# Optimization experiments

Measured on AMD Instinct MI355X. Metric: run time of the kernel, lower is better.

## Reference

```python
import jax, jax.numpy as jnp
import numpy as np

B, L, H, TE = 256, 2048, 64, 64  # batch, seq len, hidden_size, num_time_enc_dims


def _lin_init(k, out_d, in_d):
    bound = 1.0 / np.sqrt(in_d)
    kw, kb = jax.random.split(k)
    w = jax.random.uniform(kw, (out_d, in_d), jnp.float32, -bound, bound)
    b = jax.random.uniform(kb, (out_d,), jnp.float32, -bound, bound)
    return w, b


def setup_inputs() -> dict:
    key = jax.random.key(0)
    ks = jax.random.split(key, 16)
    x_xy = jax.random.normal(ks[0], (B, L, 2), jnp.float32)
    mask = jax.random.bernoulli(ks[1], 0.8, (B, L, 1)).astype(jnp.float32)  # 0 => masked position
    x = jnp.concatenate([x_xy, mask], axis=-1)  # (B,L,3)
    t = jax.random.uniform(ks[2], (B, L, 1), jnp.float32)
    te_w1, te_b1 = _lin_init(ks[3], TE, 1)
    te_w2, te_b2 = _lin_init(ks[4], TE, TE)
    fproj_w, fproj_b = _lin_init(ks[5], H, 3 + TE)
    bproj_w, bproj_b = _lin_init(ks[6], H, 3 + TE)
    fwz, fbz = _lin_init(ks[7], H, H)
    fwh, fbh = _lin_init(ks[8], H, H)
    bwz, bbz = _lin_init(ks[9], H, H)
    bwh, bbh = _lin_init(ks[10], H, H)
    head_hidden = max((2 * H + TE) // 2, 128)  # = 128
    gh_w1, gh_b1 = _lin_init(ks[11], head_hidden, 2 * H + TE)
    gh_w2, gh_b2 = _lin_init(ks[12], 1, head_hidden)
    mask_token = jnp.array([0.0, 0.01], jnp.float32) + jnp.array([0.1, 0.001], jnp.float32) * jax.random.normal(ks[13], (2,), jnp.float32)
    return dict(x=x, t=t, mask_token=mask_token,
                te_w1=te_w1, te_b1=te_b1, te_w2=te_w2, te_b2=te_b2,
                fproj_w=fproj_w, fproj_b=fproj_b, bproj_w=bproj_w, bproj_b=bproj_b,
                fwz=fwz, fbz=fbz, fwh=fwh, fbh=fbh,
                bwz=bwz, bbz=bbz, bwh=bwh, bbh=bbh,
                gh_w1=gh_w1, gh_b1=gh_b1, gh_w2=gh_w2, gh_b2=gh_b2)


def _mingru_prestates(inp, wz, bz, wh, bh, reverse):
    # inp: (B,L,H). Returns the hidden state BEFORE each step's update, in
    # time order, matching the torch code which stores h_* before cell.step.
    z = jax.nn.sigmoid(jnp.einsum('blh,oh->blo', inp, wz) + bz)
    h_tilde = jnp.tanh(jnp.einsum('blh,oh->blo', inp, wh) + bh)

    def step(h, zh):
        z_t, ht_t = zh
        return (1.0 - z_t) * h + z_t * ht_t, h  # emit pre-update carry

    h0 = jnp.zeros((inp.shape[0], wz.shape[0]), inp.dtype)
    _, hs = jax.lax.scan(step, h0,
                         (jnp.swapaxes(z, 0, 1), jnp.swapaxes(h_tilde, 0, 1)),
                         reverse=reverse)
    return jnp.swapaxes(hs, 0, 1)  # (B,L,H)


def reference(x, t, mask_token,
              te_w1, te_b1, te_w2, te_b2,
              fproj_w, fproj_b, bproj_w, bproj_b,
              fwz, fbz, fwh, fbh,
              bwz, bbz, bwh, bbh,
              gh_w1, gh_b1, gh_w2, gh_b2):
    mask_chan = x[..., 2:3]                      # (B,L,1)
    masked_pos = mask_chan == 0
    x_first2 = jnp.where(masked_pos, mask_token.reshape(1, 1, 2), x[..., :2])
    x3 = jnp.concatenate([x_first2, mask_chan], axis=-1)  # (B,L,3)

    t_enc = jax.nn.relu(jnp.einsum('blk,ok->blo', t, te_w1) + te_b1)
    t_enc = jnp.einsum('blk,ok->blo', t_enc, te_w2) + te_b2  # (B,L,TE)

    x_cat = jnp.concatenate([x3, t_enc], axis=-1)  # (B,L,3+TE)

    inp_fwd = jnp.einsum('blk,ok->blo', x_cat, fproj_w) + fproj_b
    inp_bwd = jnp.einsum('blk,ok->blo', x_cat, bproj_w) + bproj_b

    h_fwd = _mingru_prestates(inp_fwd, fwz, fbz, fwh, fbh, reverse=False)  # state after steps 0..t-1
    h_bwd = _mingru_prestates(inp_bwd, bwz, bbz, bwh, bbh, reverse=True)   # state after steps L-1..t+1

    h_fwd_final = h_fwd[:, -1:, :]  # state after steps 0..L-2
    h_bwd_final = h_bwd[:, 0:1, :]  # state after steps L-1..1

    unmasked = mask_chan > 0
    h_fwd_apply = jnp.where(unmasked, h_fwd, h_fwd_final)
    h_bwd_apply = jnp.where(unmasked, h_bwd, h_bwd_final)

    h_bi = jnp.concatenate([h_fwd_apply, h_bwd_apply, t_enc], axis=-1)  # (B,L,2H+TE)
    hid = jax.nn.relu(jnp.einsum('blk,ok->blo', h_bi, gh_w1) + gh_b1)
    preds = jnp.einsum('blk,ok->blo', hid, gh_w2) + gh_b2  # (B,L,1)
    return preds
```

## Files before the change

### kernel.cpp

```cpp
#include <hip/hip_runtime.h>
#include <stdint.h>

#define NB 256
#define NL 2048

typedef __attribute__((ext_vector_type(8))) short short8;
typedef __attribute__((ext_vector_type(4))) float f32x4;
#define MFMA16(a,b,c) __builtin_amdgcn_mfma_f32_16x16x32_bf16(a,b,c,0,0,0)

static __device__ __forceinline__ unsigned short f2bf(float f) {
    union { float f; uint32_t u; } v; v.f = f;
    uint32_t u = v.u;
    uint32_t r = u + 0x7fffu + ((u >> 16) & 1u);
    return (unsigned short)(r >> 16);
}
static __device__ __forceinline__ float bflo(uint32_t u) {
    union { uint32_t u; float f; } v; v.u = u << 16; return v.f;
}
static __device__ __forceinline__ float bfhi(uint32_t u) {
    union { uint32_t u; float f; } v; v.u = u & 0xffff0000u; return v.f;
}
#if __has_builtin(__builtin_amdgcn_cvt_pk_bf16_f32)
typedef __attribute__((ext_vector_type(2))) __bf16 bf16x2_t;
static __device__ __forceinline__ uint32_t pk2(float lo, float hi) {
    union { bf16x2_t v; uint32_t u; } c;
    c.v = __builtin_amdgcn_cvt_pk_bf16_f32(lo, hi);
    return c.u;
}
static __device__ __forceinline__ unsigned short bf1(float v) {
    union { bf16x2_t v; uint32_t u; } c;
    c.v = __builtin_amdgcn_cvt_pk_bf16_f32(v, v);
    return (unsigned short)(c.u & 0xffffu);
}
#else
static __device__ __forceinline__ uint32_t pk2(float lo, float hi) {
    return ((uint32_t)f2bf(hi) << 16) | (uint32_t)f2bf(lo);
}
static __device__ __forceinline__ unsigned short bf1(float v) { return f2bf(v); }
#endif
static __device__ __forceinline__ short8 frag8(const float* p) {
    short8 r;
#pragma unroll
    for (int j = 0; j < 8; ++j) r[j] = (short)f2bf(p[j]);
    return r;
}

static __device__ __forceinline__ void barrier_lds() {
    asm volatile("s_waitcnt lgkmcnt(0)" ::: "memory");
    __builtin_amdgcn_s_barrier();
}

#define SSTR 129

__global__ __launch_bounds__(512) void scan_fused(
    const float* __restrict__ x, const float* __restrict__ t,
    const float* __restrict__ mtok,
    const float* __restrict__ te_w1, const float* __restrict__ te_b1,
    const float* __restrict__ te_w2, const float* __restrict__ te_b2,
    const float* __restrict__ fpw, const float* __restrict__ fpb,
    const float* __restrict__ bpw, const float* __restrict__ bpb,
    const float* __restrict__ fwz, const float* __restrict__ fbz,
    const float* __restrict__ fwh, const float* __restrict__ fbh,
    const float* __restrict__ bwz, const float* __restrict__ bbz,
    const float* __restrict__ bwh, const float* __restrict__ bbh,
    int b0,
    unsigned short* __restrict__ hf, unsigned short* __restrict__ hb)
{
    __shared__ __align__(16) unsigned short s_tenc[128*72];
    __shared__ __align__(16) unsigned short s_inp[128*72];
    __shared__ uint32_t s_seg[64*SSTR];
    __shared__ float s_A[8][65], s_B[8][65];
    __shared__ float s_H[64];
    __shared__ float2 s_wb[64];

    const int rl  = blockIdx.x >> 1;
    const int dir = blockIdx.x & 1;
    const int tid = threadIdx.x;
    const int h   = tid & 63;
    const int q   = tid >> 6;
    const int lq  = h >> 4;
    const int ln  = h & 15;
    const int mq  = q >> 1;
    const int nh  = q & 1;

    const int gx = (b0 + rl) << 11;
    unsigned short* out = (dir ? hb : hf) + (size_t)rl * NL * 64;

    short8 bte[2][2];
    float bite[2];
#pragma unroll
    for (int ni = 0; ni < 2; ++ni) {
        const int nt = nh*2 + ni;
        const float* row = te_w2 + (nt*16 + ln)*64;
#pragma unroll
        for (int ks = 0; ks < 2; ++ks) bte[ni][ks] = frag8(row + lq*8 + ks*32);
        bite[ni] = te_b2[nt*16 + ln];
    }
    const float* PW = dir ? bpw : fpw;
    const float* PB = dir ? bpb : fpb;
    short8 bpj[2][3];
    float bipj[2];
#pragma unroll
    for (int ni = 0; ni < 2; ++ni) {
        const int nt = nh*2 + ni;
        const float* row = PW + (nt*16 + ln)*67;
#pragma unroll
        for (int ks = 0; ks < 2; ++ks) {
            float tmp[8];
#pragma unroll
            for (int j = 0; j < 8; ++j) tmp[j] = row[3 + lq*8 + ks*32 + j];
            bpj[ni][ks] = frag8(tmp);
        }
        {
            float tmp[8];
#pragma unroll
            for (int j = 0; j < 8; ++j) tmp[j] = (lq == 0 && j < 3) ? row[j] : 0.f;
            bpj[ni][2] = frag8(tmp);
        }
        bipj[ni] = PB[nt*16 + ln];
    }
    const float* WZ = dir ? bwz : fwz;
    const float* WH = dir ? bwh : fwh;
    const float* BZ = dir ? bbz : fbz;
    const float* BH = dir ? bbh : fbh;
    short8 bz[2][2], bh[2][2];
    float biz[2], bih[2];
#pragma unroll
    for (int ni = 0; ni < 2; ++ni) {
        const int nt = nh*2 + ni;
        const float* rz = WZ + (nt*16 + ln)*64;
        const float* rh = WH + (nt*16 + ln)*64;
#pragma unroll
        for (int ks = 0; ks < 2; ++ks) {
            bz[ni][ks] = frag8(rz + lq*8 + ks*32);
            bh[ni][ks] = frag8(rh + lq*8 + ks*32);
        }
        biz[ni] = BZ[nt*16 + ln];
        bih[ni] = BH[nt*16 + ln];
    }
    const float mt0 = mtok[0], mt1 = mtok[1];

    auto G1 = [&](const float* tvv) {
#pragma unroll
        for (int mi = 0; mi < 2; ++mi) {
            short8 a0, a1;
#pragma unroll
            for (int j = 0; j < 8; ++j) {
                const float2 wb0 = s_wb[lq*8 + j];
                const float2 wb1 = s_wb[lq*8 + 32 + j];
                a0[j] = (short)bf1(fmaxf(fmaf(tvv[mi], wb0.x, wb0.y), 0.f));
                a1[j] = (short)bf1(fmaxf(fmaf(tvv[mi], wb1.x, wb1.y), 0.f));
            }
#pragma unroll
            for (int ni = 0; ni < 2; ++ni) {
                f32x4 c = {0.f, 0.f, 0.f, 0.f};
                c = MFMA16(a0, bte[ni][0], c);
                c = MFMA16(a1, bte[ni][1], c);
                const int o = (nh*2+ni)*16 + ln;
#pragma unroll
                for (int r = 0; r < 4; ++r)
                    s_tenc[((mq*2+mi)*16 + lq*4 + r)*72 + o] = bf1(c[r] + bite[ni]);
            }
        }
    };
    auto G2 = [&](const float* xr0_, const float* xr1_, const float* xmc_) {
#pragma unroll
        for (int mi = 0; mi < 2; ++mi) {
            const int mrow = (mq*2+mi)*16 + ln;
            const short8 a0 = *(const short8*)(s_tenc + mrow*72 + lq*8);
            const short8 a1 = *(const short8*)(s_tenc + mrow*72 + lq*8 + 32);
            short8 a2 = {0,0,0,0,0,0,0,0};
            if (lq == 0) {
                const float mc  = xmc_[mi];
                const float x0m = (mc == 0.f) ? mt0 : xr0_[mi];
                const float x1m = (mc == 0.f) ? mt1 : xr1_[mi];
                a2[0] = (short)bf1(x0m);
                a2[1] = (short)bf1(x1m);
                a2[2] = (short)bf1(mc);
            }
#pragma unroll
            for (int ni = 0; ni < 2; ++ni) {
                f32x4 c = {0.f, 0.f, 0.f, 0.f};
                c = MFMA16(a0, bpj[ni][0], c);
                c = MFMA16(a1, bpj[ni][1], c);
                c = MFMA16(a2, bpj[ni][2], c);
                const int o = (nh*2+ni)*16 + ln;
#pragma unroll
                for (int r = 0; r < 4; ++r)
                    s_inp[((mq*2+mi)*16 + lq*4 + r)*72 + o] = bf1(c[r] + bipj[ni]);
            }
        }
    };
    auto GATES = [&]() {
#pragma unroll
        for (int mi = 0; mi < 2; ++mi) {
            const int mrow = (mq*2+mi)*16 + ln;
            const short8 a0 = *(const short8*)(s_inp + mrow*72 + lq*8);
            const short8 a1 = *(const short8*)(s_inp + mrow*72 + lq*8 + 32);
#pragma unroll
            for (int ni = 0; ni < 2; ++ni) {
                f32x4 cz  = {0.f, 0.f, 0.f, 0.f};
                f32x4 ch2 = {0.f, 0.f, 0.f, 0.f};
                cz  = MFMA16(a0, bz[ni][0], cz);
                cz  = MFMA16(a1, bz[ni][1], cz);
                ch2 = MFMA16(a0, bh[ni][0], ch2);
                ch2 = MFMA16(a1, bh[ni][1], ch2);
                const int hcol = (nh*2+ni)*16 + ln;
#pragma unroll
                for (int r = 0; r < 4; ++r) {
                    const float az = cz[r]  + biz[ni];
                    const float ah = ch2[r] + bih[ni];
                    const float z  = __builtin_amdgcn_rcpf(1.f + __expf(-az));
                    const float cc = fminf(fmaxf(ah, -15.f), 15.f);
                    const float e2 = __expf(2.f * cc);
                    const float th = 1.f - 2.f * __builtin_amdgcn_rcpf(e2 + 1.f);
                    s_seg[hcol*SSTR + (mq*2+mi)*16 + lq*4 + r] = pk2(1.f - z, z * th);
                }
            }
        }
    };

    if (tid < 64) {
        s_H[tid] = 0.f;
        s_wb[tid] = make_float2(te_w1[tid], te_b1[tid]);
    }
    barrier_lds();

    const int s0 = dir ? 15 : 0;
    {
        float tv0[2];
#pragma unroll
        for (int mi = 0; mi < 2; ++mi)
            tv0[mi] = t[gx + s0*128 + (mq*2+mi)*16 + ln];
        G1(tv0);
    }
    barrier_lds();
    {
        float xr0_[2], xr1_[2], xmc_[2];
        if (lq == 0) {
#pragma unroll
            for (int mi = 0; mi < 2; ++mi) {
                const float* xp = x + (size_t)(gx + s0*128 + (mq*2+mi)*16 + ln)*3;
                xr0_[mi] = xp[0]; xr1_[mi] = xp[1]; xmc_[mi] = xp[2];
            }
        }
        G2(xr0_, xr1_, xmc_);
    }
    barrier_lds();

    uint32_t regs[16];
    int l0p = 0;

#pragma unroll 1
    for (int si = 0; si < 16; ++si) {
        const int s = dir ? (15 - si) : si;
        const int sn = dir ? (14 - si) : (si + 1);
        if (si > 0) {
            float hv = s_A[q][h];
#pragma unroll
            for (int i = 0; i < 16; ++i) {
                const int g = q*16 + i;
                const int xx = dir ? (127 - g) : g;
                out[(size_t)(l0p + xx)*64 + h] = bf1(hv);
                hv = fmaf(bflo(regs[i]), hv, bfhi(regs[i]));
            }
        }
        GATES();
        barrier_lds();
        float tvn[2];
        if (si < 15) {
#pragma unroll
            for (int mi = 0; mi < 2; ++mi)
                tvn[mi] = t[gx + sn*128 + (mq*2+mi)*16 + ln];
        }
        {
            float A = 1.f, Bc = 0.f;
#pragma unroll
            for (int i = 0; i < 16; ++i) {
                const int g = q*16 + i;
                const int xx = dir ? (127 - g) : g;
                const uint32_t uab = s_seg[h*SSTR + xx];
                regs[i] = uab;
                Bc = fmaf(bflo(uab), Bc, bfhi(uab));
                A *= bflo(uab);
            }
            s_A[q][h] = A; s_B[q][h] = Bc;
        }
        if (si < 15) G1(tvn);
        barrier_lds();
        float xr0_[2], xr1_[2], xmc_[2];
        if (si < 15 && lq == 0) {
#pragma unroll
            for (int mi = 0; mi < 2; ++mi) {
                const float* xp = x + (size_t)(gx + sn*128 + (mq*2+mi)*16 + ln)*3;
                xr0_[mi] = xp[0]; xr1_[mi] = xp[1]; xmc_[mi] = xp[2];
            }
        }
        if (tid < 64) {
            float H = s_H[tid];
#pragma unroll
            for (int qq = 0; qq < 8; ++qq) {
                const float a = s_A[qq][tid], b = s_B[qq][tid];
                s_A[qq][tid] = H;
                H = fmaf(a, H, b);
            }
            s_H[tid] = H;
        }
        if (si < 15) G2(xr0_, xr1_, xmc_);
        barrier_lds();
        l0p = s * 128;
    }
    {
        float hv = s_A[q][h];
#pragma unroll
        for (int i = 0; i < 16; ++i) {
            const int g = q*16 + i;
            const int xx = dir ? (127 - g) : g;
            out[(size_t)(l0p + xx)*64 + h] = bf1(hv);
            hv = fmaf(bflo(regs[i]), hv, bfhi(regs[i]));
        }
    }
}

__global__ __launch_bounds__(256, 3) void head_kernel(
    const float* __restrict__ x, const float* __restrict__ t,
    const float* __restrict__ te_w1, const float* __restrict__ te_b1,
    const float* __restrict__ te_w2, const float* __restrict__ te_b2,
    const unsigned short* __restrict__ hf, const unsigned short* __restrict__ hb,
    const float* __restrict__ w1, const float* __restrict__ b1,
    const float* __restrict__ w2, const float* __restrict__ b2,
    int b0,
    float* __restrict__ out)
{
    __shared__ __align__(16) unsigned short s_a[64*200];
    __shared__ __align__(16) unsigned short s_te1[64*72];
    __shared__ float s_part[4][64];
    __shared__ float s_mc[64];

    const int tid = threadIdx.x;
    const int w   = tid >> 6;
    const int l   = tid & 63;
    const int lq  = l >> 4;
    const int ln  = l & 15;

    short8 bw1[2][6];
    float b1v[2], w2v[2];
#pragma unroll
    for (int p = 0; p < 2; ++p) {
        const int o = (2*w + p)*16 + ln;
        const float* row = w1 + o*192;
#pragma unroll
        for (int ks = 0; ks < 6; ++ks) bw1[p][ks] = frag8(row + lq*8 + ks*32);
        b1v[p] = b1[o];
        w2v[p] = w2[o];
    }
    short8 bte[2];
    {
        const float* row = te_w2 + (w*16 + ln)*64;
#pragma unroll
        for (int ks = 0; ks < 2; ++ks) bte[ks] = frag8(row + lq*8 + ks*32);
    }
    const float bias_te = te_b2[w*16 + ln];
    const float bias2 = b2[0];

    const int baseposl = blockIdx.x * 256;

    auto A = [&](int ch) {
        const int gbase = (b0 << 11) + baseposl + ch*64;
        if (tid < 64) s_mc[tid] = x[(size_t)(gbase + tid)*3 + 2];
        const int pos = tid & 63;
        const float tv = t[gbase + pos];
        const int k0 = (tid >> 6) * 16;
        uint32_t* dst = (uint32_t*)(s_te1 + pos*72 + k0);
#pragma unroll
        for (int kk = 0; kk < 16; kk += 2) {
            float v0 = fmaxf(fmaf(tv, te_w1[k0+kk],   te_b1[k0+kk]),   0.f);
            float v1 = fmaxf(fmaf(tv, te_w1[k0+kk+1], te_b1[k0+kk+1]), 0.f);
            dst[kk >> 1] = pk2(v0, v1);
        }
    };
    auto Bp = [&](int ch) {
        const int chbase = baseposl + ch*64;
        const int ll0 = chbase & 2047;
        const int bl  = chbase >> 11;
        const size_t rowbase = (size_t)bl * NL * 64;
#pragma unroll
        for (int rep = 0; rep < 4; ++rep) {
            const int idx = rep*256 + tid;
            const int seg = idx >> 9;
            const int row = (idx >> 3) & 63;
            const int c   = idx & 7;
            const bool unm = s_mc[row] > 0.f;
            const uint4* src = (seg == 0)
                ? (const uint4*)(hf + rowbase + (size_t)(unm ? (ll0+row) : (NL-1))*64)
                : (const uint4*)(hb + rowbase + (size_t)(unm ? (ll0+row) : 0)*64);
            ((uint4*)s_a)[row*25 + seg*8 + c] = src[c];
        }
        const int o = w*16 + ln;
#pragma unroll
        for (int mt = 0; mt < 4; ++mt) {
            f32x4 c = {0.f, 0.f, 0.f, 0.f};
#pragma unroll
            for (int ks = 0; ks < 2; ++ks) {
                const short8 a = *(const short8*)(s_te1 + (mt*16+ln)*72 + lq*8 + ks*32);
                c = MFMA16(a, bte[ks], c);
            }
#pragma unroll
            for (int r = 0; r < 4; ++r) {
                const int m = mt*16 + lq*4 + r;
                s_a[m*200 + 128 + o] = bf1(c[r] + bias_te);
            }
        }
    };
    auto Cp = [&]() {
#pragma unroll
        for (int mt = 0; mt < 4; ++mt) {
            short8 af[6];
#pragma unroll
            for (int ks = 0; ks < 6; ++ks)
                af[ks] = *(const short8*)(s_a + (mt*16+ln)*200 + lq*8 + ks*32);
            float vs[4] = {0.f, 0.f, 0.f, 0.f};
#pragma unroll
            for (int p = 0; p < 2; ++p) {
                f32x4 c = {0.f, 0.f, 0.f, 0.f};
#pragma unroll
                for (int ks = 0; ks < 6; ++ks) c = MFMA16(af[ks], bw1[p][ks], c);
#pragma unroll
                for (int r = 0; r < 4; ++r)
                    vs[r] += fmaxf(c[r] + b1v[p], 0.f) * w2v[p];
            }
#pragma unroll
            for (int mask = 1; mask < 16; mask <<= 1) {
#pragma unroll
                for (int r = 0; r < 4; ++r)
                    vs[r] += __shfl_xor(vs[r], mask);
            }
            if (ln == 0) {
#pragma unroll
                for (int r = 0; r < 4; ++r)
                    s_part[w][mt*16 + lq*4 + r] = vs[r];
            }
        }
    };
    auto Dp = [&](int ch) {
        const int gbase = (b0 << 11) + baseposl + ch*64;
        if (tid < 64) {
            out[gbase + tid] = s_part[0][tid] + s_part[1][tid]
                             + s_part[2][tid] + s_part[3][tid] + bias2;
        }
    };

    A(0);
    barrier_lds();
#pragma unroll 1
    for (int ch = 0; ch < 4; ++ch) {
        Bp(ch);
        barrier_lds();
        Cp();
        barrier_lds();
        Dp(ch);
        if (ch < 3) A(ch + 1);
        barrier_lds();
    }
}

extern "C" void kernel_launch(void* const* d_in, const int* in_sizes, int n_in,
                              void* d_out, int out_size, void* d_ws, size_t ws_size,
                              hipStream_t stream)
{
    const float* x     = (const float*)d_in[0];
    const float* t     = (const float*)d_in[1];
    const float* mtok  = (const float*)d_in[2];
    const float* te_w1 = (const float*)d_in[3];
    const float* te_b1 = (const float*)d_in[4];
    const float* te_w2 = (const float*)d_in[5];
    const float* te_b2 = (const float*)d_in[6];
    const float* fpw   = (const float*)d_in[7];
    const float* fpb   = (const float*)d_in[8];
    const float* bpw   = (const float*)d_in[9];
    const float* bpb   = (const float*)d_in[10];
    const float* fwz   = (const float*)d_in[11];
    const float* fbz   = (const float*)d_in[12];
    const float* fwh   = (const float*)d_in[13];
    const float* fbh   = (const float*)d_in[14];
    const float* bwz   = (const float*)d_in[15];
    const float* bbz   = (const float*)d_in[16];
    const float* bwh   = (const float*)d_in[17];
    const float* bbh   = (const float*)d_in[18];
    const float* w1    = (const float*)d_in[19];
    const float* b1    = (const float*)d_in[20];
    const float* w2    = (const float*)d_in[21];
    const float* b2    = (const float*)d_in[22];

    const size_t per_b = 524288ull;
    int Bg = NB;
    while ((size_t)Bg * per_b > ws_size && Bg > 1) Bg >>= 1;
    const int nG = NB / Bg;

    char* ws = (char*)d_ws;
    unsigned short* hf = (unsigned short*)ws;
    unsigned short* hb = hf + (size_t)Bg * NL * 64;

    for (int g = 0; g < nG; ++g) {
        const int b0 = g * Bg;

        scan_fused<<<2 * Bg, 512, 0, stream>>>(
            x, t, mtok, te_w1, te_b1, te_w2, te_b2,
            fpw, fpb, bpw, bpb, fwz, fbz, fwh, fbh, bwz, bbz, bwh, bbh,
            b0, hf, hb);

        head_kernel<<<8 * Bg, 256, 0, stream>>>(
            x, t, te_w1, te_b1, te_w2, te_b2,
            hf, hb, w1, b1, w2, b2, b0, (float*)d_out);
    }
}
```

Baseline: 323.0 us.

## Prefetch next chunk's hidden states into registers during head MLP compute

The head kernel now issues global loads of the next chunk's forward/backward hidden states into registers before running the MLP on the current chunk, and writes them to LDS only after that compute. The time-encoding first layer is computed directly in registers as MFMA A-fragments, so the s_te1 LDS staging buffer goes away. The mask channel for all four chunks is loaded once up front, and the per-iteration barrier count drops from three to two. The cost is more register pressure from holding prefetched uint4s, which could hurt occupancy under the launch_bounds(256,3) constraint.

After: 336.3 us. +4.1%, slower.

```diff
diff --git a/kernel.cpp b/kernel.cpp
--- a/kernel.cpp
+++ b/kernel.cpp
@@ -333,9 +333,9 @@
     float* __restrict__ out)
 {
     __shared__ __align__(16) unsigned short s_a[64*200];
-    __shared__ __align__(16) unsigned short s_te1[64*72];
     __shared__ float s_part[4][64];
-    __shared__ float s_mc[64];
+    __shared__ float s_mcall[256];
+    __shared__ float2 s_wb[64];
 
     const int tid = threadIdx.x;
     const int w   = tid >> 6;
@@ -364,22 +364,11 @@
     const float bias2 = b2[0];
 
     const int baseposl = blockIdx.x * 256;
-
-    auto A = [&](int ch) {
-        const int gbase = (b0 << 11) + baseposl + ch*64;
-        if (tid < 64) s_mc[tid] = x[(size_t)(gbase + tid)*3 + 2];
-        const int pos = tid & 63;
-        const float tv = t[gbase + pos];
-        const int k0 = (tid >> 6) * 16;
-        uint32_t* dst = (uint32_t*)(s_te1 + pos*72 + k0);
-#pragma unroll
-        for (int kk = 0; kk < 16; kk += 2) {
-            float v0 = fmaxf(fmaf(tv, te_w1[k0+kk],   te_b1[k0+kk]),   0.f);
-            float v1 = fmaxf(fmaf(tv, te_w1[k0+kk+1], te_b1[k0+kk+1]), 0.f);
-            dst[kk >> 1] = pk2(v0, v1);
-        }
-    };
-    auto Bp = [&](int ch) {
+    const int gbase0 = (b0 << 11) + baseposl;
+
+    uint4 greg[4];
+
+    auto GISSUE = [&](int ch) {
         const int chbase = baseposl + ch*64;
         const int ll0 = chbase & 2047;
         const int bl  = chbase >> 11;
@@ -390,26 +379,43 @@
             const int seg = idx >> 9;
             const int row = (idx >> 3) & 63;
             const int c   = idx & 7;
-            const bool unm = s_mc[row] > 0.f;
+            const bool unm = s_mcall[ch*64 + row] > 0.f;
             const uint4* src = (seg == 0)
                 ? (const uint4*)(hf + rowbase + (size_t)(unm ? (ll0+row) : (NL-1))*64)
                 : (const uint4*)(hb + rowbase + (size_t)(unm ? (ll0+row) : 0)*64);
-            ((uint4*)s_a)[row*25 + seg*8 + c] = src[c];
-        }
+            greg[rep] = src[c];
+        }
+    };
+    auto GWRITE = [&]() {
+#pragma unroll
+        for (int rep = 0; rep < 4; ++rep) {
+            const int idx = rep*256 + tid;
+            const int seg = idx >> 9;
+            const int row = (idx >> 3) & 63;
+            const int c   = idx & 7;
+            ((uint4*)s_a)[row*25 + seg*8 + c] = greg[rep];
+        }
+    };
+    auto TENC = [&](int ch) {
+        const int chbase = gbase0 + ch*64;
         const int o = w*16 + ln;
 #pragma unroll
         for (int mt = 0; mt < 4; ++mt) {
+            const float tv = t[chbase + mt*16 + ln];
+            short8 a0, a1;
+#pragma unroll
+            for (int j = 0; j < 8; ++j) {
+                const float2 wb0 = s_wb[lq*8 + j];
+                const float2 wb1 = s_wb[lq*8 + 32 + j];
+                a0[j] = (short)bf1(fmaxf(fmaf(tv, wb0.x, wb0.y), 0.f));
+                a1[j] = (short)bf1(fmaxf(fmaf(tv, wb1.x, wb1.y), 0.f));
+            }
             f32x4 c = {0.f, 0.f, 0.f, 0.f};
-#pragma unroll
-            for (int ks = 0; ks < 2; ++ks) {
-                const short8 a = *(const short8*)(s_te1 + (mt*16+ln)*72 + lq*8 + ks*32);
-                c = MFMA16(a, bte[ks], c);
-            }
-#pragma unroll
-            for (int r = 0; r < 4; ++r) {
-                const int m = mt*16 + lq*4 + r;
-                s_a[m*200 + 128 + o] = bf1(c[r] + bias_te);
-            }
+            c = MFMA16(a0, bte[0], c);
+            c = MFMA16(a1, bte[1], c);
+#pragma unroll
+            for (int r = 0; r < 4; ++r)
+                s_a[(mt*16 + lq*4 + r)*200 + 128 + o] = bf1(c[r] + bias_te);
         }
     };
     auto Cp = [&]() {
@@ -443,25 +449,28 @@
         }
     };
     auto Dp = [&](int ch) {
-        const int gbase = (b0 << 11) + baseposl + ch*64;
         if (tid < 64) {
-            out[gbase + tid] = s_part[0][tid] + s_part[1][tid]
-                             + s_part[2][tid] + s_part[3][tid] + bias2;
-        }
-    };
-
-    A(0);
+            out[gbase0 + ch*64 + tid] = s_part[0][tid] + s_part[1][tid]
+                                      + s_part[2][tid] + s_part[3][tid] + bias2;
+        }
+    };
+
+    s_mcall[tid] = x[(size_t)(gbase0 + tid)*3 + 2];
+    if (tid < 64) s_wb[tid] = make_float2(te_w1[tid], te_b1[tid]);
     barrier_lds();
+    GISSUE(0);
+
 #pragma unroll 1
     for (int ch = 0; ch < 4; ++ch) {
-        Bp(ch);
+        if (ch > 0) Dp(ch - 1);
+        TENC(ch);
+        GWRITE();
         barrier_lds();
+        if (ch < 3) GISSUE(ch + 1);
         Cp();
         barrier_lds();
-        Dp(ch);
-        if (ch < 3) A(ch + 1);
-        barrier_lds();
-    }
+    }
+    Dp(3);
 }
 
 extern "C" void kernel_launch(void* const* d_in, const int* in_sizes, int n_in,
```

## Fold input projection into gate weights and restructure scan chunk pipeline

Applied to the files above, without the earlier changes.

Adds a small kernel that precomputes the products of each gate weight with its direction's input projection (weights and biases), so the scan kernel computes the z and h gates directly from the concatenated features. This removes one GEMM stage, the s_inp LDS buffer and one barrier phase per chunk. The chunk loop is also reorganised: the carry combine now runs on every wave with a double-buffered s_H, outputs are written in the same iteration, and the t/x loads are prefetched two chunks ahead. The folded weights are rounded to bf16 once, which changes rounding compared with the two-stage product.

Measured after the change: 403.3 us. +24.8%, slower.

```diff
diff --git a/kernel.cpp b/kernel.cpp
--- a/kernel.cpp
+++ b/kernel.cpp
@@ -50,27 +50,50 @@
     __builtin_amdgcn_s_barrier();
 }
 
-#define SSTR 129
-
-__global__ __launch_bounds__(512) void scan_fused(
-    const float* __restrict__ x, const float* __restrict__ t,
-    const float* __restrict__ mtok,
-    const float* __restrict__ te_w1, const float* __restrict__ te_b1,
-    const float* __restrict__ te_w2, const float* __restrict__ te_b2,
+__global__ __launch_bounds__(64) void fold_weights(
     const float* __restrict__ fpw, const float* __restrict__ fpb,
     const float* __restrict__ bpw, const float* __restrict__ bpb,
     const float* __restrict__ fwz, const float* __restrict__ fbz,
     const float* __restrict__ fwh, const float* __restrict__ fbh,
     const float* __restrict__ bwz, const float* __restrict__ bbz,
     const float* __restrict__ bwh, const float* __restrict__ bbh,
+    float* __restrict__ gw, float* __restrict__ gb)
+{
+    const int combo = blockIdx.x;
+    const int o     = threadIdx.x;
+    const int dir   = combo >> 1;
+    const int gate  = combo & 1;
+    const float* W  = dir ? (gate ? bwh : bwz) : (gate ? fwh : fwz);
+    const float* Bv = dir ? (gate ? bbh : bbz) : (gate ? fbh : fbz);
+    const float* P  = dir ? bpw : fpw;
+    const float* pb = dir ? bpb : fpb;
+    float* outw = gw + (size_t)combo*64*67 + o*67;
+    for (int k = 0; k < 67; ++k) {
+        float acc = 0.f;
+        for (int j = 0; j < 64; ++j)
+            acc = fmaf(W[o*64 + j], P[j*67 + k], acc);
+        outw[k] = acc;
+    }
+    float accb = Bv[o];
+    for (int j = 0; j < 64; ++j) accb = fmaf(W[o*64 + j], pb[j], accb);
+    gb[combo*64 + o] = accb;
+}
+
+#define SSTR 129
+
+__global__ __launch_bounds__(512) void scan_fused(
+    const float* __restrict__ x, const float* __restrict__ t,
+    const float* __restrict__ mtok,
+    const float* __restrict__ te_w1, const float* __restrict__ te_b1,
+    const float* __restrict__ te_w2, const float* __restrict__ te_b2,
+    const float* __restrict__ gw, const float* __restrict__ gb,
     int b0,
     unsigned short* __restrict__ hf, unsigned short* __restrict__ hb)
 {
     __shared__ __align__(16) unsigned short s_tenc[128*72];
-    __shared__ __align__(16) unsigned short s_inp[128*72];
     __shared__ uint32_t s_seg[64*SSTR];
     __shared__ float s_A[8][65], s_B[8][65];
-    __shared__ float s_H[64];
+    __shared__ float s_H[2][64];
     __shared__ float2 s_wb[64];
 
     const int rl  = blockIdx.x >> 1;
@@ -96,47 +119,40 @@
         for (int ks = 0; ks < 2; ++ks) bte[ni][ks] = frag8(row + lq*8 + ks*32);
         bite[ni] = te_b2[nt*16 + ln];
     }
-    const float* PW = dir ? bpw : fpw;
-    const float* PB = dir ? bpb : fpb;
-    short8 bpj[2][3];
-    float bipj[2];
+    const float* GZ  = gw + (size_t)(dir*2 + 0)*64*67;
+    const float* GH  = gw + (size_t)(dir*2 + 1)*64*67;
+    const float* BZ2 = gb + (dir*2 + 0)*64;
+    const float* BH2 = gb + (dir*2 + 1)*64;
+    short8 bgz[2][3], bgh[2][3];
+    float biz[2], bih[2];
 #pragma unroll
     for (int ni = 0; ni < 2; ++ni) {
         const int nt = nh*2 + ni;
-        const float* row = PW + (nt*16 + ln)*67;
+        const float* rz = GZ + (nt*16 + ln)*67;
+        const float* rh = GH + (nt*16 + ln)*67;
 #pragma unroll
         for (int ks = 0; ks < 2; ++ks) {
-            float tmp[8];
-#pragma unroll
-            for (int j = 0; j < 8; ++j) tmp[j] = row[3 + lq*8 + ks*32 + j];
-            bpj[ni][ks] = frag8(tmp);
+            float tz[8], th[8];
+#pragma unroll
+            for (int j = 0; j < 8; ++j) {
+                tz[j] = rz[3 + lq*8 + ks*32 + j];
+                th[j] = rh[3 + lq*8 + ks*32 + j];
+            }
+            bgz[ni][ks] = frag8(tz);
+            bgh[ni][ks] = frag8(th);
         }
         {
-            float tmp[8];
-#pragma unroll
-            for (int j = 0; j < 8; ++j) tmp[j] = (lq == 0 && j < 3) ? row[j] : 0.f;
-            bpj[ni][2] = frag8(tmp);
-        }
-        bipj[ni] = PB[nt*16 + ln];
-    }
-    const float* WZ = dir ? bwz : fwz;
-    const float* WH = dir ? bwh : fwh;
-    const float* BZ = dir ? bbz : fbz;
-    const float* BH = dir ? bbh : fbh;
-    short8 bz[2][2], bh[2][2];
-    float biz[2], bih[2];
-#pragma unroll
-    for (int ni = 0; ni < 2; ++ni) {
-        const int nt = nh*2 + ni;
-        const float* rz = WZ + (nt*16 + ln)*64;
-        const float* rh = WH + (nt*16 + ln)*64;
-#pragma unroll
-        for (int ks = 0; ks < 2; ++ks) {
-            bz[ni][ks] = frag8(rz + lq*8 + ks*32);
-            bh[ni][ks] = frag8(rh + lq*8 + ks*32);
-        }
-        biz[ni] = BZ[nt*16 + ln];
-        bih[ni] = BH[nt*16 + ln];
+            float tz[8], th[8];
+#pragma unroll
+            for (int j = 0; j < 8; ++j) {
+                tz[j] = (lq == 0 && j < 3) ? rz[j] : 0.f;
+                th[j] = (lq == 0 && j < 3) ? rh[j] : 0.f;
+            }
+            bgz[ni][2] = frag8(tz);
+            bgh[ni][2] = frag8(th);
+        }
+        biz[ni] = BZ2[nt*16 + ln];
+        bih[ni] = BH2[nt*16 + ln];
     }
     const float mt0 = mtok[0], mt1 = mtok[1];
 
@@ -163,7 +179,7 @@
             }
         }
     };
-    auto G2 = [&](const float* xr0_, const float* xr1_, const float* xmc_) {
+    auto GZH = [&](const float* xr0_, const float* xr1_, const float* xmc_) {
 #pragma unroll
         for (int mi = 0; mi < 2; ++mi) {
             const int mrow = (mq*2+mi)*16 + ln;
@@ -180,31 +196,14 @@
             }
 #pragma unroll
             for (int ni = 0; ni < 2; ++ni) {
-                f32x4 c = {0.f, 0.f, 0.f, 0.f};
-                c = MFMA16(a0, bpj[ni][0], c);
-                c = MFMA16(a1, bpj[ni][1], c);
-                c = MFMA16(a2, bpj[ni][2], c);
-                const int o = (nh*2+ni)*16 + ln;
-#pragma unroll
-                for (int r = 0; r < 4; ++r)
-                    s_inp[((mq*2+mi)*16 + lq*4 + r)*72 + o] = bf1(c[r] + bipj[ni]);
-            }
-        }
-    };
-    auto GATES = [&]() {
-#pragma unroll
-        for (int mi = 0; mi < 2; ++mi) {
-            const int mrow = (mq*2+mi)*16 + ln;
-            const short8 a0 = *(const short8*)(s_inp + mrow*72 + lq*8);
-            const short8 a1 = *(const short8*)(s_inp + mrow*72 + lq*8 + 32);
-#pragma unroll
-            for (int ni = 0; ni < 2; ++ni) {
                 f32x4 cz  = {0.f, 0.f, 0.f, 0.f};
                 f32x4 ch2 = {0.f, 0.f, 0.f, 0.f};
-                cz  = MFMA16(a0, bz[ni][0], cz);
-                cz  = MFMA16(a1, bz[ni][1], cz);
-                ch2 = MFMA16(a0, bh[ni][0], ch2);
-                ch2 = MFMA16(a1, bh[ni][1], ch2);
+                cz  = MFMA16(a0, bgz[ni][0], cz);
+                cz  = MFMA16(a1, bgz[ni][1], cz);
+                cz  = MFMA16(a2, bgz[ni][2], cz);
+                ch2 = MFMA16(a0, bgh[ni][0], ch2);
+                ch2 = MFMA16(a1, bgh[ni][1], ch2);
+                ch2 = MFMA16(a2, bgh[ni][2], ch2);
                 const int hcol = (nh*2+ni)*16 + ln;
 #pragma unroll
                 for (int r = 0; r < 4; ++r) {
@@ -221,12 +220,13 @@
     };
 
     if (tid < 64) {
-        s_H[tid] = 0.f;
+        s_H[0][tid] = 0.f;
         s_wb[tid] = make_float2(te_w1[tid], te_b1[tid]);
     }
     barrier_lds();
 
     const int s0 = dir ? 15 : 0;
+    const int s1 = dir ? 14 : 1;
     {
         float tv0[2];
 #pragma unroll
@@ -234,45 +234,35 @@
             tv0[mi] = t[gx + s0*128 + (mq*2+mi)*16 + ln];
         G1(tv0);
     }
+    float xr0_[2], xr1_[2], xmc_[2];
+    if (lq == 0) {
+#pragma unroll
+        for (int mi = 0; mi < 2; ++mi) {
+            const float* xp = x + (size_t)(gx + s0*128 + (mq*2+mi)*16 + ln)*3;
+            xr0_[mi] = xp[0]; xr1_[mi] = xp[1]; xmc_[mi] = xp[2];
+        }
+    }
     barrier_lds();
-    {
-        float xr0_[2], xr1_[2], xmc_[2];
-        if (lq == 0) {
-#pragma unroll
-            for (int mi = 0; mi < 2; ++mi) {
-                const float* xp = x + (size_t)(gx + s0*128 + (mq*2+mi)*16 + ln)*3;
-                xr0_[mi] = xp[0]; xr1_[mi] = xp[1]; xmc_[mi] = xp[2];
-            }
-        }
-        G2(xr0_, xr1_, xmc_);
+    GZH(xr0_, xr1_, xmc_);
+    float tvn[2];
+#pragma unroll
+    for (int mi = 0; mi < 2; ++mi)
+        tvn[mi] = t[gx + s1*128 + (mq*2+mi)*16 + ln];
+    if (lq == 0) {
+#pragma unroll
+        for (int mi = 0; mi < 2; ++mi) {
+            const float* xp = x + (size_t)(gx + s1*128 + (mq*2+mi)*16 + ln)*3;
+            xr0_[mi] = xp[0]; xr1_[mi] = xp[1]; xmc_[mi] = xp[2];
+        }
     }
     barrier_lds();
 
     uint32_t regs[16];
-    int l0p = 0;
+    int p = 0;
 
 #pragma unroll 1
     for (int si = 0; si < 16; ++si) {
-        const int s = dir ? (15 - si) : si;
-        const int sn = dir ? (14 - si) : (si + 1);
-        if (si > 0) {
-            float hv = s_A[q][h];
-#pragma unroll
-            for (int i = 0; i < 16; ++i) {
-                const int g = q*16 + i;
-                const int xx = dir ? (127 - g) : g;
-                out[(size_t)(l0p + xx)*64 + h] = bf1(hv);
-                hv = fmaf(bflo(regs[i]), hv, bfhi(regs[i]));
-            }
-        }
-        GATES();
-        barrier_lds();
-        float tvn[2];
-        if (si < 15) {
-#pragma unroll
-            for (int mi = 0; mi < 2; ++mi)
-                tvn[mi] = t[gx + sn*128 + (mq*2+mi)*16 + ln];
-        }
+        const int s  = dir ? (15 - si) : si;
         {
             float A = 1.f, Bc = 0.f;
 #pragma unroll
@@ -288,37 +278,45 @@
         }
         if (si < 15) G1(tvn);
         barrier_lds();
-        float xr0_[2], xr1_[2], xmc_[2];
-        if (si < 15 && lq == 0) {
-#pragma unroll
-            for (int mi = 0; mi < 2; ++mi) {
-                const float* xp = x + (size_t)(gx + sn*128 + (mq*2+mi)*16 + ln)*3;
-                xr0_[mi] = xp[0]; xr1_[mi] = xp[1]; xmc_[mi] = xp[2];
-            }
-        }
-        if (tid < 64) {
-            float H = s_H[tid];
+        float Hin;
+        {
+            float H = s_H[p][h];
 #pragma unroll
             for (int qq = 0; qq < 8; ++qq) {
-                const float a = s_A[qq][tid], b = s_B[qq][tid];
-                s_A[qq][tid] = H;
-                H = fmaf(a, H, b);
-            }
-            s_H[tid] = H;
-        }
-        if (si < 15) G2(xr0_, xr1_, xmc_);
+                if (qq == q) Hin = H;
+                H = fmaf(s_A[qq][h], H, s_B[qq][h]);
+            }
+            if (q == 0) s_H[p ^ 1][h] = H;
+        }
+        p ^= 1;
+        {
+            const int l0 = s * 128;
+            float hv = Hin;
+#pragma unroll
+            for (int i = 0; i < 16; ++i) {
+                const int g = q*16 + i;
+                const int xx = dir ? (127 - g) : g;
+                out[(size_t)(l0 + xx)*64 + h] = bf1(hv);
+                hv = fmaf(bflo(regs[i]), hv, bfhi(regs[i]));
+            }
+        }
+        if (si < 15) {
+            GZH(xr0_, xr1_, xmc_);
+            if (si < 14) {
+                const int s2 = dir ? (13 - si) : (si + 2);
+#pragma unroll
+                for (int mi = 0; mi < 2; ++mi)
+                    tvn[mi] = t[gx + s2*128 + (mq*2+mi)*16 + ln];
+                if (lq == 0) {
+#pragma unroll
+                    for (int mi = 0; mi < 2; ++mi) {
+                        const float* xp = x + (size_t)(gx + s2*128 + (mq*2+mi)*16 + ln)*3;
+                        xr0_[mi] = xp[0]; xr1_[mi] = xp[1]; xmc_[mi] = xp[2];
+                    }
+                }
+            }
+        }
         barrier_lds();
-        l0p = s * 128;
-    }
-    {
-        float hv = s_A[q][h];
-#pragma unroll
-        for (int i = 0; i < 16; ++i) {
-            const int g = q*16 + i;
-            const int xx = dir ? (127 - g) : g;
-            out[(size_t)(l0p + xx)*64 + h] = bf1(hv);
-            hv = fmaf(bflo(regs[i]), hv, bfhi(regs[i]));
-        }
     }
 }
 
@@ -492,22 +490,27 @@
     const float* w2    = (const float*)d_in[21];
     const float* b2    = (const float*)d_in[22];
 
+    const size_t tail  = (size_t)4*64*67*4 + (size_t)4*64*4;
     const size_t per_b = 524288ull;
     int Bg = NB;
-    while ((size_t)Bg * per_b > ws_size && Bg > 1) Bg >>= 1;
+    while ((size_t)Bg * per_b + tail > ws_size && Bg > 1) Bg >>= 1;
     const int nG = NB / Bg;
 
     char* ws = (char*)d_ws;
     unsigned short* hf = (unsigned short*)ws;
     unsigned short* hb = hf + (size_t)Bg * NL * 64;
+    float* gw = (float*)(hb + (size_t)Bg * NL * 64);
+    float* gb = gw + (size_t)4*64*67;
+
+    fold_weights<<<4, 64, 0, stream>>>(
+        fpw, fpb, bpw, bpb, fwz, fbz, fwh, fbh, bwz, bbz, bwh, bbh, gw, gb);
 
     for (int g = 0; g < nG; ++g) {
         const int b0 = g * Bg;
 
         scan_fused<<<2 * Bg, 512, 0, stream>>>(
             x, t, mtok, te_w1, te_b1, te_w2, te_b2,
-            fpw, fpb, bpw, bpb, fwz, fbz, fwh, fbh, bwz, bbz, bwh, bbh,
-            b0, hf, hb);
+            gw, gb, b0, hf, hb);
 
         head_kernel<<<8 * Bg, 256, 0, stream>>>(
             x, t, te_w1, te_b1, te_w2, te_b2,
```
